# Performance work log

Hardware: AMD Instinct MI355X
Metric: run time of the kernel (lower is better)

## Reference

```python
import jax, jax.numpy as jnp
import numpy as np

H = 512  # hidden_size


def setup_inputs() -> dict:
    key = jax.random.key(0)
    ks = jax.random.split(key, 8)
    B, L_tgt, L_src = 4, 32, 1024
    query = jax.random.normal(ks[0], (B, L_tgt, H), dtype=jnp.float32)
    states = jax.random.normal(ks[1], (B, L_src, 2 * H), dtype=jnp.float32)
    source_mask = jnp.ones((B, L_src), dtype=jnp.int32)
    s = 0.02
    Wq = jax.random.normal(ks[2], (H, 2 * H), dtype=jnp.float32) * s      # _linear_query.weight^T
    bq = jax.random.normal(ks[3], (2 * H,), dtype=jnp.float32) * s        # _linear_query.bias
    Ws = jax.random.normal(ks[4], (2 * H, 2 * H), dtype=jnp.float32) * s  # _linear_source.weight^T (no bias)
    v = jax.random.normal(ks[5], (2 * H,), dtype=jnp.float32) * s         # _v.weight (no bias)
    Wc = jax.random.normal(ks[6], (3 * H, H), dtype=jnp.float32) * s      # _context.weight^T
    bc = jax.random.normal(ks[7], (H,), dtype=jnp.float32) * s            # _context.bias
    return {"query": query, "states": states, "source_mask": source_mask,
            "Wq": Wq, "bq": bq, "Ws": Ws, "v": v, "Wc": Wc, "bc": bc}


def reference(query, states, source_mask, Wq, bq, Ws, v, Wc, bc):
    # Bahdanau additive attention.
    # query: (B, T, H), states: (B, S, 2H), source_mask: (B, S)
    qf = query @ Wq + bq                         # (B, T, 2H)
    sf = states @ Ws                             # (B, S, 2H)
    # alignments: v . tanh(qf[:, :, None] + sf[:, None, :])  -> (B, T, S)
    feats = jnp.tanh(qf[:, :, None, :] + sf[:, None, :, :])  # (B, T, S, 2H)
    alignments = jnp.einsum('btsd,d->bts', feats, v)
    # mask (B, S) -> (B, 1, S); masked positions get -inf before softmax
    alignments = jnp.where(source_mask[:, None, :].astype(bool), alignments, -jnp.inf)
    attentions = jax.nn.softmax(alignments, axis=2)           # (B, T, S)
    context = jnp.einsum('bts,bsd->btd', attentions, states)  # (B, T, 2H)
    concat_context = jnp.concatenate((context, query), axis=2)  # (B, T, 3H)
    attention_hidden = concat_context @ Wc + bc               # (B, T, H)
    attentions_t = jnp.swapaxes(attentions, 1, 2)             # (B, S, T)
    return (context, attention_hidden, attentions_t)
```

## Files before the change

### kernel.cpp

```cpp
#include <hip/hip_runtime.h>
#include <math.h>


typedef unsigned short u16;
typedef __bf16 bf16x8 __attribute__((ext_vector_type(8)));
typedef float floatx4 __attribute__((ext_vector_type(4)));

#define B_ 4
#define T_ 32
#define S_ 1024
#define H_ 512
#define D_ 1024
#define BT_ 128
#define TWO_LOG2E 2.8853900817779268f
#define LOG2E 1.4426950408889634f

__device__ __forceinline__ float bf2f(u16 u) {
  unsigned int i = ((unsigned int)u) << 16;
  return __builtin_bit_cast(float, i);
}
__device__ __forceinline__ u16 f2bf(float f) {
  unsigned int i = __builtin_bit_cast(unsigned int, f);
  i += 0x7fffu + ((i >> 16) & 1u);
  return (u16)(i >> 16);
}
__device__ __forceinline__ void ld_g2l_16(const u16* g, u16* l) {
  __builtin_amdgcn_global_load_lds((__attribute__((address_space(1))) void*)(u16*)g,
                                   (__attribute__((address_space(3))) void*)l, 16, 0, 0);
}


__global__ __launch_bounds__(256) void prep_fused4(const float* __restrict__ states, const float* __restrict__ Ws,
                                                   const float* __restrict__ query, const float* __restrict__ Wq,
                                                   const float* __restrict__ bq,
                                                   u16* __restrict__ sbf, u16* __restrict__ sbfT,
                                                   u16* __restrict__ WsT, float* __restrict__ qfp,
                                                   float* __restrict__ rowsum) {
  __shared__ u16 tile[32][65];
  __shared__ float q[8][128];
  const int t = threadIdx.x;
  if (blockIdx.x < 512) {
    if (blockIdx.x == 0 && t < 128) rowsum[t] = 0.f;
    const int n0 = (blockIdx.x & 15) * 64, k0 = (blockIdx.x >> 4) * 32;
    const int kr = t >> 3, nc = (t & 7) * 8;
    const float* p = Ws + (size_t)(k0 + kr) * D_ + n0 + nc;
    float4 a = *(const float4*)p, b = *(const float4*)(p + 4);
    tile[kr][nc + 0] = f2bf(a.x); tile[kr][nc + 1] = f2bf(a.y);
    tile[kr][nc + 2] = f2bf(a.z); tile[kr][nc + 3] = f2bf(a.w);
    tile[kr][nc + 4] = f2bf(b.x); tile[kr][nc + 5] = f2bf(b.y);
    tile[kr][nc + 6] = f2bf(b.z); tile[kr][nc + 7] = f2bf(b.w);
    __syncthreads();
    const int nr = t >> 2, kc = (t & 3) * 8;
    union { uint4 v; u16 s[8]; } st;
#pragma unroll
    for (int i = 0; i < 8; ++i) st.s[i] = tile[kc + i][nr];
    *(uint4*)(WsT + (size_t)(n0 + nr) * D_ + k0 + kc) = st.v;
  } else if (blockIdx.x < 2560) {
    const int bid = blockIdx.x - 512;
    const int b = bid >> 9;
    const int r2 = bid & 511;
    const int d0 = (r2 & 15) * 64, s0 = (r2 >> 4) * 32;
    const int sr = t >> 3, dc = (t & 7) * 8;
    const float* p = states + ((size_t)b * S_ + s0 + sr) * D_ + d0 + dc;
    float4 a = *(const float4*)p, bb = *(const float4*)(p + 4);
    union { uint4 v; u16 s[8]; } pk;
    pk.s[0] = f2bf(a.x); pk.s[1] = f2bf(a.y); pk.s[2] = f2bf(a.z); pk.s[3] = f2bf(a.w);
    pk.s[4] = f2bf(bb.x); pk.s[5] = f2bf(bb.y); pk.s[6] = f2bf(bb.z); pk.s[7] = f2bf(bb.w);
    *(uint4*)(sbf + ((size_t)b * S_ + s0 + sr) * D_ + d0 + dc) = pk.v;
#pragma unroll
    for (int i = 0; i < 8; ++i) tile[sr][dc + i] = pk.s[i];
    __syncthreads();
    const int dr = t >> 2, sc = (t & 3) * 8;
    union { uint4 v; u16 s[8]; } st;
#pragma unroll
    for (int i = 0; i < 8; ++i) st.s[i] = tile[sc + i][dr];
    *(uint4*)(sbfT + ((size_t)b * D_ + d0 + dr) * S_ + s0 + sc) = st.v;
  } else {
    const int idx = blockIdx.x - 2560;
    const int c0 = (idx & 3) * 256, r0 = ((idx >> 2) & 15) * 8, ks = idx >> 6;
    const int k0 = ks * 128;
    for (int i = t; i < 8 * 128; i += 256) {
      const int rl = i >> 7, kk = i & 127;
      q[rl][kk] = query[(size_t)(r0 + rl) * H_ + k0 + kk];
    }
    __syncthreads();
    const int col = c0 + t;
    float acc[8] = {};
    for (int kk = 0; kk < 128; ++kk) {
      const float w = Wq[(size_t)(k0 + kk) * D_ + col];
#pragma unroll
      for (int r = 0; r < 8; ++r) acc[r] = fmaf(q[r][kk], w, acc[r]);
    }
    const float bb = (ks == 0) ? bq[col] : 0.f;
    float* dst = qfp + (size_t)ks * (BT_ * D_);
#pragma unroll
    for (int r = 0; r < 8; ++r)
      dst[(size_t)(r0 + r) * D_ + col] = TWO_LOG2E * (acc[r] + bb);
  }
}

__device__ __forceinline__ void f2f_stage(const u16* __restrict__ A, const u16* __restrict__ BT,
                                          u16* sAb, u16* sBb, int bm0, int bn0, int k0,
                                          int wv, int srow, int sp) {
#pragma unroll
  for (int j = 0; j < 4; ++j) {
    const int r = wv * 32 + j * 8 + srow;
    const int c = sp ^ (r & 7);
    ld_g2l_16(A + (size_t)(bm0 + r) * D_ + k0 + c * 8, sAb + (wv * 32 + j * 8) * 64);
  }
#pragma unroll
  for (int j = 0; j < 2; ++j) {
    const int r = wv * 16 + j * 8 + srow;
    const int c = sp ^ (r & 7);
    ld_g2l_16(BT + (size_t)(bn0 + r) * D_ + k0 + c * 8, sBb + (wv * 16 + j * 8) * 64);
  }
}

__device__ __forceinline__ void f2f_compute(const u16* sAb, const u16* sBb,
                                            int wm, int wn, int fm, int fq, floatx4 (&acc)[4][2]) {
#pragma unroll
  for (int win = 0; win < 2; ++win) {
    bf16x8 af[4], bfr[2];
#pragma unroll
    for (int i = 0; i < 4; ++i) {
      const int R = wm + i * 16 + fm;
      af[i] = *(const bf16x8*)&sAb[R * 64 + ((win * 4 + fq) ^ (R & 7)) * 8];
    }
#pragma unroll
    for (int j = 0; j < 2; ++j) {
      const int R = wn + j * 16 + fm;
      bfr[j] = *(const bf16x8*)&sBb[R * 64 + ((win * 4 + fq) ^ (R & 7)) * 8];
    }
#pragma unroll
    for (int i = 0; i < 4; ++i)
#pragma unroll
      for (int j = 0; j < 2; ++j)
        acc[i][j] = __builtin_amdgcn_mfma_f32_16x16x32_bf16(af[i], bfr[j], acc[i][j], 0, 0, 0);
  }
}

__global__ __launch_bounds__(256) void f2i_sfgemm(const u16* __restrict__ A, const u16* __restrict__ BT,
                                                  const float* __restrict__ qfp, float* __restrict__ Eq,
                                                  u16* __restrict__ Es) {
  __shared__ __align__(16) u16 sA[2][128 * 64];
  __shared__ __align__(16) u16 sB[2][64 * 64];
  const int bm0 = blockIdx.y * 128, bn0 = blockIdx.x * 64;
  const int t = threadIdx.x;
  const int wv = t >> 6, lane = t & 63;
  const int wm = (wv >> 1) * 64, wn = (wv & 1) * 32;
  const int fm = lane & 15, fq = lane >> 4;
  const int srow = lane >> 3, sp = lane & 7;

  {
    const int bid = blockIdx.y * 16 + blockIdx.x;
    const int idx = bid * 256 + t;
    const float s = qfp[idx] + qfp[BT_ * D_ + idx] +
                    qfp[2 * BT_ * D_ + idx] + qfp[3 * BT_ * D_ + idx];
    Eq[idx] = __builtin_amdgcn_exp2f(s);
  }

  floatx4 acc[4][2];
  const floatx4 fz = {0.f, 0.f, 0.f, 0.f};
#pragma unroll
  for (int i = 0; i < 4; ++i) { acc[i][0] = fz; acc[i][1] = fz; }

  f2f_stage(A, BT, sA[0], sB[0], bm0, bn0, 0, wv, srow, sp);
#pragma unroll 1
  for (int k0 = 0; k0 < D_; k0 += 128) {
    f2f_stage(A, BT, sA[1], sB[1], bm0, bn0, k0 + 64, wv, srow, sp);
    asm volatile("s_waitcnt vmcnt(6)" ::: "memory");
    __builtin_amdgcn_s_barrier();
    f2f_compute(sA[0], sB[0], wm, wn, fm, fq, acc);
    __builtin_amdgcn_s_barrier();
    if (k0 + 128 < D_) {
      f2f_stage(A, BT, sA[0], sB[0], bm0, bn0, k0 + 128, wv, srow, sp);
      asm volatile("s_waitcnt vmcnt(6)" ::: "memory");
    } else {
      asm volatile("s_waitcnt vmcnt(0)" ::: "memory");
    }
    __builtin_amdgcn_s_barrier();
    f2f_compute(sA[1], sB[1], wm, wn, fm, fq, acc);
    __builtin_amdgcn_s_barrier();
  }
#pragma unroll
  for (int i = 0; i < 4; ++i)
#pragma unroll
    for (int j = 0; j < 2; ++j)
#pragma unroll
      for (int r = 0; r < 4; ++r) {
        const int row = bm0 + wm + i * 16 + fq * 4 + r;
        const int col = bn0 + wn + j * 16 + fm;
        Es[(size_t)row * D_ + col] = f2bf(__builtin_amdgcn_exp2f(TWO_LOG2E * acc[i][j][r]));
      }
}

__global__ __launch_bounds__(256) void f3i_align(const float* __restrict__ Eq, const u16* __restrict__ Es,
                                                 const float* __restrict__ v, const int* __restrict__ mask,
                                                 u16* __restrict__ pbf, float* __restrict__ rowsum) {
  __shared__ float red[32][4];
  const int wid = (blockIdx.x * 256 + threadIdx.x) >> 6;
  const int lane = threadIdx.x & 63;
  const int wv = threadIdx.x >> 6;
  const int b = wid >> 10, s = wid & 1023;
  const int msk = mask[(size_t)b * S_ + s];
  float vm2[16], es[16];
  float sumv = 0.f;
  {
    union { uint4 u[2]; u16 h[16]; } ue;
    const uint4* ep = (const uint4*)(Es + (size_t)wid * D_ + lane * 16);
    ue.u[0] = ep[0]; ue.u[1] = ep[1];
    const float4* vp = (const float4*)(v + lane * 16);
#pragma unroll
    for (int c = 0; c < 4; ++c) {
      const float4 w4 = vp[c];
      vm2[4 * c + 0] = -2.f * w4.x; vm2[4 * c + 1] = -2.f * w4.y;
      vm2[4 * c + 2] = -2.f * w4.z; vm2[4 * c + 3] = -2.f * w4.w;
      sumv += w4.x + w4.y + w4.z + w4.w;
    }
#pragma unroll
    for (int j = 0; j < 16; ++j) es[j] = bf2f(ue.h[j]);
  }
  const float* qbase = Eq + ((size_t)(b * T_)) * D_ + lane * 16;
  for (int tc = 0; tc < 8; ++tc) {
    float sum[4];
#pragma unroll
    for (int ti = 0; ti < 4; ++ti) {
      const float4* qp = (const float4*)(qbase + (size_t)(tc * 4 + ti) * D_);
      float acc = sumv;
#pragma unroll
      for (int c = 0; c < 4; ++c) {
        const float4 q4 = qp[c];
        const float xs[4] = {q4.x, q4.y, q4.z, q4.w};
#pragma unroll
        for (int u2 = 0; u2 < 4; ++u2) {
          const int j = 4 * c + u2;
          acc = fmaf(vm2[j], __builtin_amdgcn_rcpf(fmaf(xs[u2], es[j], 1.f)), acc);
        }
      }
      sum[ti] = acc;
    }
#pragma unroll
    for (int off = 32; off > 0; off >>= 1)
#pragma unroll
      for (int ti = 0; ti < 4; ++ti) sum[ti] += __shfl_xor(sum[ti], off);
    if (lane == 0) {
#pragma unroll
      for (int ti = 0; ti < 4; ++ti) {
        const int tt = tc * 4 + ti;
        const float e = msk ? __builtin_amdgcn_exp2f(sum[ti] * LOG2E) : 0.f;
        const u16 pe = f2bf(e);
        pbf[((size_t)(b * T_ + tt)) * S_ + s] = pe;
        red[tt][wv] = bf2f(pe);
      }
    }
  }
  __syncthreads();
  if (threadIdx.x < 32) {
    const int bb = blockIdx.x >> 8;
    const float rs = red[threadIdx.x][0] + red[threadIdx.x][1] +
                     red[threadIdx.x][2] + red[threadIdx.x][3];
    atomicAdd(&rowsum[bb * 32 + threadIdx.x], rs);
  }
}

__global__ __launch_bounds__(256) void f5d_context(const u16* __restrict__ pbf, const u16* __restrict__ sbfT,
                                                   const float* __restrict__ rowsum,
                                                   float* __restrict__ ctx, float* __restrict__ out_at) {
  __shared__ float rinv[32];
  const int b = blockIdx.x >> 4, dt = blockIdx.x & 15;
  if (threadIdx.x < 32) rinv[threadIdx.x] = 1.f / rowsum[b * 32 + threadIdx.x];
  __syncthreads();
  const int wv = threadIdx.x >> 6, lane = threadIdx.x & 63;
  const int n0 = dt * 64 + wv * 16;
  const int fm = lane & 15, fq = lane >> 4;
  const floatx4 fz = {0.f, 0.f, 0.f, 0.f};
  floatx4 acc0 = fz, acc1 = fz;
  const u16* pa0 = pbf + ((size_t)b * T_ + fm) * S_ + fq * 8;
  const u16* pa1 = pbf + ((size_t)b * T_ + 16 + fm) * S_ + fq * 8;
  const u16* pb  = sbfT + ((size_t)b * D_ + n0 + fm) * S_ + fq * 8;
#pragma unroll 4
  for (int k0 = 0; k0 < S_; k0 += 32) {
    bf16x8 a0 = *(const bf16x8*)(pa0 + k0);
    bf16x8 a1 = *(const bf16x8*)(pa1 + k0);
    bf16x8 bb = *(const bf16x8*)(pb + k0);
    acc0 = __builtin_amdgcn_mfma_f32_16x16x32_bf16(a0, bb, acc0, 0, 0, 0);
    acc1 = __builtin_amdgcn_mfma_f32_16x16x32_bf16(a1, bb, acc1, 0, 0, 0);
  }
  const int col = n0 + fm;
#pragma unroll
  for (int r = 0; r < 4; ++r) {
    const int t0r = fq * 4 + r;
    ctx[((size_t)b * T_ + t0r) * D_ + col] = acc0[r] * rinv[t0r];
    ctx[((size_t)b * T_ + 16 + t0r) * D_ + col] = acc1[r] * rinv[16 + t0r];
  }
  const int s0 = dt * 64;
  for (int i = threadIdx.x; i < 64 * 32; i += 256) {
    const int tt = i >> 6, sl = i & 63;
    const float e = bf2f(pbf[((size_t)(b * T_ + tt)) * S_ + s0 + sl]);
    out_at[((size_t)(b * S_ + s0 + sl)) * T_ + tt] = e * rinv[tt];
  }
}

__global__ __launch_bounds__(256) void f6b_outproj(const float* __restrict__ ctx, const float* __restrict__ query,
                                                   const float* __restrict__ Wc, const float* __restrict__ bc,
                                                   float* __restrict__ out_hid) {
  __shared__ float cq[16][128];
  const int c0 = blockIdx.x * 128, r0 = blockIdx.y * 16, k0 = blockIdx.z * 128;
  const int tid = threadIdx.x;
  const int cl = tid & 127, rh = tid >> 7;
  for (int i = tid; i < 16 * 128; i += 256) {
    const int rl = i >> 7, kk = i & 127;
    const int k = k0 + kk, row = r0 + rl;
    cq[rl][kk] = (k < D_) ? ctx[(size_t)row * D_ + k] : query[(size_t)row * H_ + k - D_];
  }
  __syncthreads();
  float acc[8] = {};
  for (int kk = 0; kk < 128; ++kk) {
    const float w = Wc[(size_t)(k0 + kk) * H_ + c0 + cl];
#pragma unroll
    for (int rr = 0; rr < 8; ++rr) acc[rr] = fmaf(cq[rh * 8 + rr][kk], w, acc[rr]);
  }
  const float bb = (blockIdx.z == 0) ? bc[c0 + cl] : 0.f;
#pragma unroll
  for (int rr = 0; rr < 8; ++rr)
    atomicAdd(&out_hid[(size_t)(r0 + rh * 8 + rr) * H_ + c0 + cl], acc[rr] + bb);
}


__global__ __launch_bounds__(256) void prep_fused(const float* __restrict__ states, const float* __restrict__ Ws,
                                                  const float* __restrict__ query, const float* __restrict__ Wq,
                                                  const float* __restrict__ bq,
                                                  u16* __restrict__ sbf, u16* __restrict__ sbfT,
                                                  u16* __restrict__ WsT, float* __restrict__ qf) {
  __shared__ u16 tile[32][65];
  __shared__ float q[8][128];
  const int t = threadIdx.x;
  if (blockIdx.x < 512) {
    const int n0 = (blockIdx.x & 15) * 64, k0 = (blockIdx.x >> 4) * 32;
    const int kr = t >> 3, nc = (t & 7) * 8;
    const float* p = Ws + (size_t)(k0 + kr) * D_ + n0 + nc;
    float4 a = *(const float4*)p, b = *(const float4*)(p + 4);
    tile[kr][nc + 0] = f2bf(a.x); tile[kr][nc + 1] = f2bf(a.y);
    tile[kr][nc + 2] = f2bf(a.z); tile[kr][nc + 3] = f2bf(a.w);
    tile[kr][nc + 4] = f2bf(b.x); tile[kr][nc + 5] = f2bf(b.y);
    tile[kr][nc + 6] = f2bf(b.z); tile[kr][nc + 7] = f2bf(b.w);
    __syncthreads();
    const int nr = t >> 2, kc = (t & 3) * 8;
    union { uint4 v; u16 s[8]; } st;
#pragma unroll
    for (int i = 0; i < 8; ++i) st.s[i] = tile[kc + i][nr];
    *(uint4*)(WsT + (size_t)(n0 + nr) * D_ + k0 + kc) = st.v;
  } else if (blockIdx.x < 2560) {
    const int bid = blockIdx.x - 512;
    const int b = bid >> 9;
    const int r2 = bid & 511;
    const int d0 = (r2 & 15) * 64, s0 = (r2 >> 4) * 32;
    const int sr = t >> 3, dc = (t & 7) * 8;
    const float* p = states + ((size_t)b * S_ + s0 + sr) * D_ + d0 + dc;
    float4 a = *(const float4*)p, bb = *(const float4*)(p + 4);
    union { uint4 v; u16 s[8]; } pk;
    pk.s[0] = f2bf(a.x); pk.s[1] = f2bf(a.y); pk.s[2] = f2bf(a.z); pk.s[3] = f2bf(a.w);
    pk.s[4] = f2bf(bb.x); pk.s[5] = f2bf(bb.y); pk.s[6] = f2bf(bb.z); pk.s[7] = f2bf(bb.w);
    *(uint4*)(sbf + ((size_t)b * S_ + s0 + sr) * D_ + d0 + dc) = pk.v;
#pragma unroll
    for (int i = 0; i < 8; ++i) tile[sr][dc + i] = pk.s[i];
    __syncthreads();
    const int dr = t >> 2, sc = (t & 3) * 8;
    union { uint4 v; u16 s[8]; } st;
#pragma unroll
    for (int i = 0; i < 8; ++i) st.s[i] = tile[sc + i][dr];
    *(uint4*)(sbfT + ((size_t)b * D_ + d0 + dr) * S_ + s0 + sc) = st.v;
  } else {
    const int idx = blockIdx.x - 2560;
    const int c0 = (idx & 3) * 256, r0 = ((idx >> 2) & 15) * 8, k0 = (idx >> 6) * 128;
    for (int i = t; i < 8 * 128; i += 256) {
      const int rl = i >> 7, kk = i & 127;
      q[rl][kk] = query[(size_t)(r0 + rl) * H_ + k0 + kk];
    }
    __syncthreads();
    const int col = c0 + t;
    float acc[8] = {};
    for (int kk = 0; kk < 128; ++kk) {
      const float w = Wq[(size_t)(k0 + kk) * D_ + col];
#pragma unroll
      for (int r = 0; r < 8; ++r) acc[r] = fmaf(q[r][kk], w, acc[r]);
    }
    const float bb = (k0 == 0) ? bq[col] : 0.f;
#pragma unroll
    for (int r = 0; r < 8; ++r)
      atomicAdd(&qf[(size_t)(r0 + r) * D_ + col], TWO_LOG2E * (acc[r] + bb));
  }
}

__global__ __launch_bounds__(256) void f2e_sfgemm(const u16* __restrict__ A, const u16* __restrict__ BT,
                                                  u16* __restrict__ Cb) {
  __shared__ __align__(16) u16 sA[128 * 64];
  __shared__ __align__(16) u16 sB[64 * 64];
  const int bm0 = blockIdx.y * 128, bn0 = blockIdx.x * 64;
  const int t = threadIdx.x;
  const int wv = t >> 6, lane = t & 63;
  const int wm = (wv >> 1) * 64, wn = (wv & 1) * 32;
  const int fm = lane & 15, fq = lane >> 4;
  const int srow = lane >> 3, sp = lane & 7;

  floatx4 acc[4][2];
  const floatx4 fz = {0.f, 0.f, 0.f, 0.f};
#pragma unroll
  for (int i = 0; i < 4; ++i) { acc[i][0] = fz; acc[i][1] = fz; }

  for (int k0 = 0; k0 < D_; k0 += 64) {
    __syncthreads();
#pragma unroll
    for (int j = 0; j < 4; ++j) {
      const int r = wv * 32 + j * 8 + srow;
      const int c = sp ^ (r & 7);
      ld_g2l_16(A + (size_t)(bm0 + r) * D_ + k0 + c * 8, &sA[(wv * 32 + j * 8) * 64]);
    }
#pragma unroll
    for (int j = 0; j < 2; ++j) {
      const int r = wv * 16 + j * 8 + srow;
      const int c = sp ^ (r & 7);
      ld_g2l_16(BT + (size_t)(bn0 + r) * D_ + k0 + c * 8, &sB[(wv * 16 + j * 8) * 64]);
    }
    __syncthreads();
#pragma unroll
    for (int win = 0; win < 2; ++win) {
      bf16x8 af[4], bfr[2];
#pragma unroll
      for (int i = 0; i < 4; ++i) {
        const int R = wm + i * 16 + fm;
        af[i] = *(const bf16x8*)&sA[R * 64 + ((win * 4 + fq) ^ (R & 7)) * 8];
      }
#pragma unroll
      for (int j = 0; j < 2; ++j) {
        const int R = wn + j * 16 + fm;
        bfr[j] = *(const bf16x8*)&sB[R * 64 + ((win * 4 + fq) ^ (R & 7)) * 8];
      }
#pragma unroll
      for (int i = 0; i < 4; ++i)
#pragma unroll
        for (int j = 0; j < 2; ++j)
          acc[i][j] = __builtin_amdgcn_mfma_f32_16x16x32_bf16(af[i], bfr[j], acc[i][j], 0, 0, 0);
    }
  }
#pragma unroll
  for (int i = 0; i < 4; ++i)
#pragma unroll
    for (int j = 0; j < 2; ++j)
#pragma unroll
      for (int r = 0; r < 4; ++r) {
        const int row = bm0 + wm + i * 16 + fq * 4 + r;
        const int col = bn0 + wn + j * 16 + fm;
        Cb[(size_t)row * D_ + col] = f2bf(TWO_LOG2E * acc[i][j][r]);
      }
}

__global__ __launch_bounds__(256, 6) void f3f_align(const float* __restrict__ qf, const u16* __restrict__ sfb,
                                                    const float* __restrict__ v, float* __restrict__ alg) {
  const int wid = (blockIdx.x * 256 + threadIdx.x) >> 6;
  const int lane = threadIdx.x & 63;
  const int b = wid >> 10, s = wid & 1023;
  const int t0 = blockIdx.y * 16;
  float vr[16], sr[16];
  {
    union { uint4 v[2]; u16 s[16]; } u;
    const uint4* sp = (const uint4*)(sfb + (size_t)wid * D_ + lane * 16);
    u.v[0] = sp[0]; u.v[1] = sp[1];
    const float* vp = v + lane * 16;
#pragma unroll
    for (int c = 0; c < 4; ++c) {
      float4 w = *(const float4*)(vp + 4 * c);
      vr[4 * c + 0] = w.x; vr[4 * c + 1] = w.y; vr[4 * c + 2] = w.z; vr[4 * c + 3] = w.w;
    }
#pragma unroll
    for (int j = 0; j < 16; ++j) sr[j] = bf2f(u.s[j]);
  }
  float sum[16];
#pragma unroll
  for (int tt = 0; tt < 16; ++tt) sum[tt] = 0.f;

  const float* qbase = qf + ((size_t)(b * T_ + t0)) * D_ + lane * 16;
  for (int tt = 0; tt < 16; ++tt) {
    const float4* qp = (const float4*)(qbase + (size_t)tt * D_);
    float acc = 0.f;
#pragma unroll
    for (int c = 0; c < 4; ++c) {
      float4 q4 = qp[c];
      float xs[4] = {q4.x, q4.y, q4.z, q4.w};
#pragma unroll
      for (int u2 = 0; u2 < 4; ++u2) {
        const int j = 4 * c + u2;
        const float x = xs[u2] + sr[j];
        const float e = __builtin_amdgcn_exp2f(x);
        acc = fmaf(vr[j], fmaf(-2.f, __builtin_amdgcn_rcpf(e + 1.f), 1.f), acc);
      }
    }
    sum[tt] = acc;
  }
#pragma unroll
  for (int off = 32; off > 0; off >>= 1)
#pragma unroll
    for (int tt = 0; tt < 16; ++tt) sum[tt] += __shfl_xor(sum[tt], off);
  if (lane == 0) {
#pragma unroll
    for (int tt = 0; tt < 16; ++tt)
      alg[((size_t)(b * T_ + t0 + tt)) * S_ + s] = sum[tt];
  }
}

__global__ __launch_bounds__(256) void f4b_softmax(const float* __restrict__ alg, const int* __restrict__ mask,
                                                   float* __restrict__ out_at, u16* __restrict__ pbf) {
  const int r = blockIdx.x;
  const int b = r >> 5, t = r & 31;
  const int tid = threadIdx.x;
  __shared__ float red[256];
  float a[4];
#pragma unroll
  for (int jj = 0; jj < 4; ++jj) {
    const int s = tid + 256 * jj;
    const float x = alg[(size_t)r * S_ + s];
    a[jj] = (mask[(size_t)b * S_ + s] != 0) ? x : -3.0e38f;
  }
  float m = fmaxf(fmaxf(a[0], a[1]), fmaxf(a[2], a[3]));
  red[tid] = m; __syncthreads();
  for (int st = 128; st > 0; st >>= 1) { if (tid < st) red[tid] = fmaxf(red[tid], red[tid + st]); __syncthreads(); }
  m = red[0]; __syncthreads();
  float e[4], lsum = 0.f;
#pragma unroll
  for (int jj = 0; jj < 4; ++jj) {
    e[jj] = (a[jj] > -1.0e38f) ? expf(a[jj] - m) : 0.f;
    lsum += e[jj];
  }
  red[tid] = lsum; __syncthreads();
  for (int st = 128; st > 0; st >>= 1) { if (tid < st) red[tid] += red[tid + st]; __syncthreads(); }
  const float rs = 1.f / red[0];
#pragma unroll
  for (int jj = 0; jj < 4; ++jj) {
    const int s = tid + 256 * jj;
    const float p = e[jj] * rs;
    out_at[((size_t)b * S_ + s) * T_ + t] = p;
    pbf[(size_t)r * S_ + s] = f2bf(p);
  }
}

__global__ __launch_bounds__(256) void f5c_context(const u16* __restrict__ pbf, const u16* __restrict__ sbfT,
                                                   float* __restrict__ ctx) {
  const int b = blockIdx.x >> 4, dt = blockIdx.x & 15;
  const int wv = threadIdx.x >> 6, lane = threadIdx.x & 63;
  const int n0 = dt * 64 + wv * 16;
  const int fm = lane & 15, fq = lane >> 4;
  const floatx4 fz = {0.f, 0.f, 0.f, 0.f};
  floatx4 acc0 = fz, acc1 = fz;
  const u16* pa0 = pbf + ((size_t)b * T_ + fm) * S_ + fq * 8;
  const u16* pa1 = pbf + ((size_t)b * T_ + 16 + fm) * S_ + fq * 8;
  const u16* pb  = sbfT + ((size_t)b * D_ + n0 + fm) * S_ + fq * 8;
#pragma unroll 4
  for (int k0 = 0; k0 < S_; k0 += 32) {
    bf16x8 a0 = *(const bf16x8*)(pa0 + k0);
    bf16x8 a1 = *(const bf16x8*)(pa1 + k0);
    bf16x8 bb = *(const bf16x8*)(pb + k0);
    acc0 = __builtin_amdgcn_mfma_f32_16x16x32_bf16(a0, bb, acc0, 0, 0, 0);
    acc1 = __builtin_amdgcn_mfma_f32_16x16x32_bf16(a1, bb, acc1, 0, 0, 0);
  }
  const int col = n0 + fm;
#pragma unroll
  for (int r = 0; r < 4; ++r) {
    ctx[((size_t)b * T_ + fq * 4 + r) * D_ + col] = acc0[r];
    ctx[((size_t)b * T_ + 16 + fq * 4 + r) * D_ + col] = acc1[r];
  }
}


__global__ __launch_bounds__(256) void kc_cvt(const float* __restrict__ in, u16* __restrict__ out) {
  const size_t i0 = ((size_t)blockIdx.x * 256 + threadIdx.x) * 8;
  float4 a = *(const float4*)(in + i0);
  float4 b = *(const float4*)(in + i0 + 4);
  union { uint4 v; u16 s[8]; } r;
  r.s[0] = f2bf(a.x); r.s[1] = f2bf(a.y); r.s[2] = f2bf(a.z); r.s[3] = f2bf(a.w);
  r.s[4] = f2bf(b.x); r.s[5] = f2bf(b.y); r.s[6] = f2bf(b.z); r.s[7] = f2bf(b.w);
  *(uint4*)(out + i0) = r.v;
}

__global__ __launch_bounds__(256) void f0_transpose(const float* __restrict__ Ws, u16* __restrict__ WsT) {
  __shared__ u16 tile[32][65];
  const int n0 = blockIdx.x * 64, k0 = blockIdx.y * 32;
  const int t = threadIdx.x;
  {
    const int kr = t >> 3, nc = (t & 7) * 8;
    const float* p = Ws + (size_t)(k0 + kr) * D_ + n0 + nc;
    float4 a = *(const float4*)p, b = *(const float4*)(p + 4);
    tile[kr][nc + 0] = f2bf(a.x); tile[kr][nc + 1] = f2bf(a.y);
    tile[kr][nc + 2] = f2bf(a.z); tile[kr][nc + 3] = f2bf(a.w);
    tile[kr][nc + 4] = f2bf(b.x); tile[kr][nc + 5] = f2bf(b.y);
    tile[kr][nc + 6] = f2bf(b.z); tile[kr][nc + 7] = f2bf(b.w);
  }
  __syncthreads();
  {
    const int nr = t >> 2, kc = (t & 3) * 8;
    union { uint4 v; u16 s[8]; } st;
#pragma unroll
    for (int i = 0; i < 8; ++i) st.s[i] = tile[kc + i][nr];
    *(uint4*)(WsT + (size_t)(n0 + nr) * D_ + k0 + kc) = st.v;
  }
}

__global__ __launch_bounds__(256) void f1b_qf(const float* __restrict__ query, const float* __restrict__ Wq,
                                              const float* __restrict__ bq, float* __restrict__ qf) {
  __shared__ float q[8][128];
  const int c0 = blockIdx.x * 256, r0 = blockIdx.y * 8, k0 = blockIdx.z * 128;
  const int tid = threadIdx.x;
  for (int i = tid; i < 8 * 128; i += 256) {
    const int rl = i >> 7, kk = i & 127;
    q[rl][kk] = query[(size_t)(r0 + rl) * H_ + k0 + kk];
  }
  __syncthreads();
  const int col = c0 + tid;
  float acc[8] = {};
  for (int kk = 0; kk < 128; ++kk) {
    const float w = Wq[(size_t)(k0 + kk) * D_ + col];
#pragma unroll
    for (int r = 0; r < 8; ++r) acc[r] = fmaf(q[r][kk], w, acc[r]);
  }
  const float bb = (blockIdx.z == 0) ? bq[col] : 0.f;
#pragma unroll
  for (int r = 0; r < 8; ++r)
    atomicAdd(&qf[(size_t)(r0 + r) * D_ + col], TWO_LOG2E * (acc[r] + bb));
}

__global__ __launch_bounds__(256) void f2c_sfgemm(const u16* __restrict__ A, const u16* __restrict__ BT,
                                                  u16* __restrict__ Cb) {
  __shared__ __align__(16) u16 sA[128 * 40];
  __shared__ __align__(16) u16 sB[64 * 40];
  const int bm0 = blockIdx.y * 128, bn0 = blockIdx.x * 64;
  const int t = threadIdx.x;
  const int wv = t >> 6, lane = t & 63;
  const int wm = (wv >> 1) * 64, wn = (wv & 1) * 32;
  const int fm = lane & 15, fq = lane >> 4;
  const int arow = t >> 1, akc = (t & 1) * 16;
  const int brow = t >> 2, bkc = (t & 3) * 8;
  floatx4 acc[4][2];
  const floatx4 fz = {0.f, 0.f, 0.f, 0.f};
#pragma unroll
  for (int i = 0; i < 4; ++i) { acc[i][0] = fz; acc[i][1] = fz; }
  const uint4* gA = (const uint4*)(A + (size_t)(bm0 + arow) * D_ + akc);
  const uint4* gB = (const uint4*)(BT + (size_t)(bn0 + brow) * D_ + bkc);
  for (int k0 = 0; k0 < D_; k0 += 32) {
    uint4 va0 = gA[k0 >> 3];
    uint4 va1 = gA[(k0 >> 3) + 1];
    uint4 vb = gB[k0 >> 3];
    __syncthreads();
    *(uint4*)&sA[arow * 40 + akc] = va0;
    *(uint4*)&sA[arow * 40 + akc + 8] = va1;
    *(uint4*)&sB[brow * 40 + bkc] = vb;
    __syncthreads();
    bf16x8 af[4], bfr[2];
#pragma unroll
    for (int i = 0; i < 4; ++i) af[i] = *(const bf16x8*)&sA[(wm + i * 16 + fm) * 40 + fq * 8];
#pragma unroll
    for (int j = 0; j < 2; ++j) bfr[j] = *(const bf16x8*)&sB[(wn + j * 16 + fm) * 40 + fq * 8];
#pragma unroll
    for (int i = 0; i < 4; ++i)
#pragma unroll
      for (int j = 0; j < 2; ++j)
        acc[i][j] = __builtin_amdgcn_mfma_f32_16x16x32_bf16(af[i], bfr[j], acc[i][j], 0, 0, 0);
  }
#pragma unroll
  for (int i = 0; i < 4; ++i)
#pragma unroll
    for (int j = 0; j < 2; ++j)
#pragma unroll
      for (int r = 0; r < 4; ++r) {
        const int row = bm0 + wm + i * 16 + fq * 4 + r;
        const int col = bn0 + wn + j * 16 + fm;
        Cb[(size_t)row * D_ + col] = f2bf(TWO_LOG2E * acc[i][j][r]);
      }
}

__global__ __launch_bounds__(256) void f2d_sfgemm(const float* __restrict__ A, const u16* __restrict__ BT,
                                                  u16* __restrict__ Cb) {
  __shared__ __align__(16) u16 sA[128 * 40];
  __shared__ __align__(16) u16 sB[64 * 40];
  const int bm0 = blockIdx.y * 128, bn0 = blockIdx.x * 64;
  const int t = threadIdx.x;
  const int wv = t >> 6, lane = t & 63;
  const int wm = (wv >> 1) * 64, wn = (wv & 1) * 32;
  const int fm = lane & 15, fq = lane >> 4;
  const int arow = t >> 1, akc = (t & 1) * 16;
  const int brow = t >> 2, bkc = (t & 3) * 8;
  floatx4 acc[4][2];
  const floatx4 fz = {0.f, 0.f, 0.f, 0.f};
#pragma unroll
  for (int i = 0; i < 4; ++i) { acc[i][0] = fz; acc[i][1] = fz; }
  const float* gA = A + (size_t)(bm0 + arow) * D_ + akc;
  const uint4* gB = (const uint4*)(BT + (size_t)(bn0 + brow) * D_ + bkc);
  for (int k0 = 0; k0 < D_; k0 += 32) {
    float4 a0 = *(const float4*)(gA + k0);
    float4 a1 = *(const float4*)(gA + k0 + 4);
    float4 a2 = *(const float4*)(gA + k0 + 8);
    float4 a3 = *(const float4*)(gA + k0 + 12);
    uint4 vb = gB[k0 >> 3];
    union { uint4 v[2]; u16 s[16]; } pa;
    pa.s[0] = f2bf(a0.x); pa.s[1] = f2bf(a0.y); pa.s[2] = f2bf(a0.z); pa.s[3] = f2bf(a0.w);
    pa.s[4] = f2bf(a1.x); pa.s[5] = f2bf(a1.y); pa.s[6] = f2bf(a1.z); pa.s[7] = f2bf(a1.w);
    pa.s[8] = f2bf(a2.x); pa.s[9] = f2bf(a2.y); pa.s[10] = f2bf(a2.z); pa.s[11] = f2bf(a2.w);
    pa.s[12] = f2bf(a3.x); pa.s[13] = f2bf(a3.y); pa.s[14] = f2bf(a3.z); pa.s[15] = f2bf(a3.w);
    __syncthreads();
    *(uint4*)&sA[arow * 40 + akc] = pa.v[0];
    *(uint4*)&sA[arow * 40 + akc + 8] = pa.v[1];
    *(uint4*)&sB[brow * 40 + bkc] = vb;
    __syncthreads();
    bf16x8 af[4], bfr[2];
#pragma unroll
    for (int i = 0; i < 4; ++i) af[i] = *(const bf16x8*)&sA[(wm + i * 16 + fm) * 40 + fq * 8];
#pragma unroll
    for (int j = 0; j < 2; ++j) bfr[j] = *(const bf16x8*)&sB[(wn + j * 16 + fm) * 40 + fq * 8];
#pragma unroll
    for (int i = 0; i < 4; ++i)
#pragma unroll
      for (int j = 0; j < 2; ++j)
        acc[i][j] = __builtin_amdgcn_mfma_f32_16x16x32_bf16(af[i], bfr[j], acc[i][j], 0, 0, 0);
  }
#pragma unroll
  for (int i = 0; i < 4; ++i)
#pragma unroll
    for (int j = 0; j < 2; ++j)
#pragma unroll
      for (int r = 0; r < 4; ++r) {
        const int row = bm0 + wm + i * 16 + fq * 4 + r;
        const int col = bn0 + wn + j * 16 + fm;
        Cb[(size_t)row * D_ + col] = f2bf(TWO_LOG2E * acc[i][j][r]);
      }
}

__global__ __launch_bounds__(256) void f4_softmax(const float* __restrict__ alg, const int* __restrict__ mask,
                                                  float* __restrict__ attn) {
  const int r = blockIdx.x;
  const int b = r >> 5;
  const int tid = threadIdx.x;
  __shared__ float red[256];
  float a[4];
#pragma unroll
  for (int jj = 0; jj < 4; ++jj) {
    const int s = tid + 256 * jj;
    const float x = alg[(size_t)r * S_ + s];
    a[jj] = (mask[(size_t)b * S_ + s] != 0) ? x : -3.0e38f;
  }
  float m = fmaxf(fmaxf(a[0], a[1]), fmaxf(a[2], a[3]));
  red[tid] = m; __syncthreads();
  for (int st = 128; st > 0; st >>= 1) { if (tid < st) red[tid] = fmaxf(red[tid], red[tid + st]); __syncthreads(); }
  m = red[0]; __syncthreads();
  float e[4], lsum = 0.f;
#pragma unroll
  for (int jj = 0; jj < 4; ++jj) {
    e[jj] = (a[jj] > -1.0e38f) ? expf(a[jj] - m) : 0.f;
    lsum += e[jj];
  }
  red[tid] = lsum; __syncthreads();
  for (int st = 128; st > 0; st >>= 1) { if (tid < st) red[tid] += red[tid + st]; __syncthreads(); }
  const float rs = 1.f / red[0];
#pragma unroll
  for (int jj = 0; jj < 4; ++jj)
    attn[(size_t)r * S_ + tid + 256 * jj] = e[jj] * rs;
}

__global__ __launch_bounds__(256) void f5b_context(const float* __restrict__ attn, const u16* __restrict__ sbf,
                                                   float* __restrict__ ctx, float* __restrict__ out_at) {
  __shared__ float at[16][64];
  const int s0 = blockIdx.x * 64, t0 = blockIdx.y * 16, b = blockIdx.z;
  const int tid = threadIdx.x;
  for (int i = tid; i < 16 * 64; i += 256) {
    const int tl = i >> 6, sl = i & 63;
    at[tl][sl] = attn[(size_t)(b * T_ + t0 + tl) * S_ + s0 + sl];
  }
  __syncthreads();
  for (int i = tid; i < 64 * 16; i += 256) {
    const int sl = i >> 4, tl = i & 15;
    out_at[((size_t)b * S_ + s0 + sl) * T_ + t0 + tl] = at[tl][sl];
  }
  float acc[16][4] = {};
  for (int sl = 0; sl < 64; ++sl) {
    const u16* srow = sbf + ((size_t)b * S_ + s0 + sl) * D_ + tid;
    float sv[4];
#pragma unroll
    for (int jj = 0; jj < 4; ++jj) sv[jj] = bf2f(srow[256 * jj]);
#pragma unroll
    for (int tl = 0; tl < 16; ++tl) {
      const float w = at[tl][sl];
#pragma unroll
      for (int jj = 0; jj < 4; ++jj) acc[tl][jj] = fmaf(w, sv[jj], acc[tl][jj]);
    }
  }
#pragma unroll
  for (int tl = 0; tl < 16; ++tl)
#pragma unroll
    for (int jj = 0; jj < 4; ++jj)
      atomicAdd(&ctx[(size_t)(b * T_ + t0 + tl) * D_ + tid + 256 * jj], acc[tl][jj]);
}

__global__ __launch_bounds__(256) void f5_context(const float* __restrict__ attn, const float* __restrict__ states,
                                                  float* __restrict__ ctx, float* __restrict__ out_at) {
  __shared__ float at[16][64];
  const int s0 = blockIdx.x * 64, t0 = blockIdx.y * 16, b = blockIdx.z;
  const int tid = threadIdx.x;
  for (int i = tid; i < 16 * 64; i += 256) {
    const int tl = i >> 6, sl = i & 63;
    at[tl][sl] = attn[(size_t)(b * T_ + t0 + tl) * S_ + s0 + sl];
  }
  __syncthreads();
  for (int i = tid; i < 64 * 16; i += 256) {
    const int sl = i >> 4, tl = i & 15;
    out_at[((size_t)b * S_ + s0 + sl) * T_ + t0 + tl] = at[tl][sl];
  }
  float acc[16][4] = {};
  for (int sl = 0; sl < 64; ++sl) {
    const float* srow = states + ((size_t)b * S_ + s0 + sl) * D_ + tid;
    float sv[4];
#pragma unroll
    for (int jj = 0; jj < 4; ++jj) sv[jj] = srow[256 * jj];
#pragma unroll
    for (int tl = 0; tl < 16; ++tl) {
      const float w = at[tl][sl];
#pragma unroll
      for (int jj = 0; jj < 4; ++jj) acc[tl][jj] = fmaf(w, sv[jj], acc[tl][jj]);
    }
  }
#pragma unroll
  for (int tl = 0; tl < 16; ++tl)
#pragma unroll
    for (int jj = 0; jj < 4; ++jj)
      atomicAdd(&ctx[(size_t)(b * T_ + t0 + tl) * D_ + tid + 256 * jj], acc[tl][jj]);
}


__global__ __launch_bounds__(256) void k1_qf(const float* __restrict__ query, const float* __restrict__ Wq,
                                             const float* __restrict__ bq, float* __restrict__ qf) {
  const int r = blockIdx.x;
  const int tid = threadIdx.x;
  __shared__ float q[H_];
  for (int i = tid; i < H_; i += 256) q[i] = query[(size_t)r * H_ + i];
  __syncthreads();
#pragma unroll
  for (int jj = 0; jj < 4; ++jj) {
    const int j = tid + 256 * jj;
    float acc = bq[j];
    for (int k = 0; k < H_; ++k) acc = fmaf(q[k], Wq[(size_t)k * D_ + j], acc);
    qf[(size_t)r * D_ + j] = acc;
  }
}

__global__ __launch_bounds__(256) void k23_align(const float* __restrict__ states, const float* __restrict__ Ws,
                                                 const float* __restrict__ v, const float* __restrict__ qf,
                                                 float* __restrict__ alg) {
  const int b = blockIdx.x >> 6;
  const int s0 = (blockIdx.x & 63) * 16;
  const int tid = threadIdx.x, lane = tid & 63, wv = tid >> 6;
  __shared__ u16 stL[16 * D_];
  __shared__ float vvL[D_];
  __shared__ float red[16 * 4];
  for (int i = tid; i < 16 * D_; i += 256) {
    const int row = i >> 10, col = i & (D_ - 1);
    stL[i] = f2bf(states[((size_t)b * S_ + s0 + row) * D_ + col]);
  }
  for (int i = tid; i < D_; i += 256) vvL[i] = v[i];
  __syncthreads();
  float acc[64];
#pragma unroll
  for (int i = 0; i < 64; ++i) acc[i] = 0.f;
#pragma unroll 4
  for (int k = 0; k < D_; ++k) {
    float wsv[4];
#pragma unroll
    for (int jj = 0; jj < 4; ++jj) wsv[jj] = Ws[(size_t)k * D_ + tid + 256 * jj];
#pragma unroll
    for (int i = 0; i < 16; ++i) {
      const float sv = bf2f(stL[i * D_ + k]);
#pragma unroll
      for (int jj = 0; jj < 4; ++jj) acc[i * 4 + jj] = fmaf(sv, wsv[jj], acc[i * 4 + jj]);
    }
  }
  for (int t = 0; t < T_; ++t) {
    float qv[4];
#pragma unroll
    for (int jj = 0; jj < 4; ++jj) qv[jj] = qf[((size_t)b * T_ + t) * D_ + tid + 256 * jj];
    float part[16];
#pragma unroll
    for (int i = 0; i < 16; ++i) {
      float p = 0.f;
#pragma unroll
      for (int jj = 0; jj < 4; ++jj)
        p = fmaf(vvL[tid + 256 * jj], tanhf(qv[jj] + acc[i * 4 + jj]), p);
      part[i] = p;
    }
#pragma unroll
    for (int i = 0; i < 16; ++i) {
      float x = part[i];
#pragma unroll
      for (int off = 32; off > 0; off >>= 1) x += __shfl_xor(x, off);
      if (lane == 0) red[i * 4 + wv] = x;
    }
    __syncthreads();
    if (tid < 16)
      alg[((size_t)b * T_ + t) * S_ + s0 + tid] =
          red[tid * 4 + 0] + red[tid * 4 + 1] + red[tid * 4 + 2] + red[tid * 4 + 3];
    __syncthreads();
  }
}

__global__ __launch_bounds__(256) void k4_softmax(const float* __restrict__ alg, const int* __restrict__ mask,
                                                  float* __restrict__ attn) {
  const int r = blockIdx.x;
  const int b = r >> 5;
  const int tid = threadIdx.x;
  __shared__ float red[256];
  float a[4];
#pragma unroll
  for (int jj = 0; jj < 4; ++jj) {
    const int s = tid + 256 * jj;
    const float x = alg[(size_t)r * S_ + s];
    a[jj] = (mask[(size_t)b * S_ + s] != 0) ? x : -3.0e38f;
  }
  float m = fmaxf(fmaxf(a[0], a[1]), fmaxf(a[2], a[3]));
  red[tid] = m; __syncthreads();
  for (int st = 128; st > 0; st >>= 1) { if (tid < st) red[tid] = fmaxf(red[tid], red[tid + st]); __syncthreads(); }
  m = red[0]; __syncthreads();
  float e[4], lsum = 0.f;
#pragma unroll
  for (int jj = 0; jj < 4; ++jj) {
    e[jj] = (a[jj] > -1.0e38f) ? expf(a[jj] - m) : 0.f;
    lsum += e[jj];
  }
  red[tid] = lsum; __syncthreads();
  for (int st = 128; st > 0; st >>= 1) { if (tid < st) red[tid] += red[tid + st]; __syncthreads(); }
  const float rs = 1.f / red[0];
#pragma unroll
  for (int jj = 0; jj < 4; ++jj)
    attn[(size_t)r * S_ + tid + 256 * jj] = e[jj] * rs;
}

__global__ __launch_bounds__(256) void k56_ctx_proj(const float* __restrict__ attn, const float* __restrict__ states,
                                                    const float* __restrict__ query, const float* __restrict__ Wc,
                                                    const float* __restrict__ bc,
                                                    float* __restrict__ out_ctx, float* __restrict__ out_hid,
                                                    float* __restrict__ out_at) {
  const int r = blockIdx.x;
  const int b = r >> 5, t = r & (T_ - 1);
  const int tid = threadIdx.x;
  __shared__ float pr[S_];
  __shared__ float cq[D_ + H_];
  for (int s = tid; s < S_; s += 256) pr[s] = attn[(size_t)r * S_ + s];
  __syncthreads();
  for (int s = tid; s < S_; s += 256) out_at[((size_t)b * S_ + s) * T_ + t] = pr[s];
  float acc[4] = {0.f, 0.f, 0.f, 0.f};
  for (int s = 0; s < S_; ++s) {
    const float w = pr[s];
    const float* srow = states + ((size_t)b * S_ + s) * D_ + tid;
#pragma unroll
    for (int jj = 0; jj < 4; ++jj) acc[jj] = fmaf(w, srow[256 * jj], acc[jj]);
  }
#pragma unroll
  for (int jj = 0; jj < 4; ++jj) {
    cq[tid + 256 * jj] = acc[jj];
    out_ctx[(size_t)r * D_ + tid + 256 * jj] = acc[jj];
  }
  for (int i = tid; i < H_; i += 256) cq[D_ + i] = query[(size_t)r * H_ + i];
  __syncthreads();
#pragma unroll
  for (int jj = 0; jj < 2; ++jj) {
    const int n = tid + 256 * jj;
    float h = bc[n];
    for (int k = 0; k < D_ + H_; ++k) h = fmaf(cq[k], Wc[(size_t)k * H_ + n], h);
    out_hid[(size_t)r * H_ + n] = h;
  }
}

extern "C" void kernel_launch(void* const* d_in, const int* in_sizes, int n_in,
                              void* d_out, int out_size, void* d_ws, size_t ws_size,
                              hipStream_t stream) {
  const float* query  = (const float*)d_in[0];
  const float* states = (const float*)d_in[1];
  const int*   mask   = (const int*)d_in[2];
  const float* Wq     = (const float*)d_in[3];
  const float* bq     = (const float*)d_in[4];
  const float* Ws     = (const float*)d_in[5];
  const float* v      = (const float*)d_in[6];
  const float* Wc     = (const float*)d_in[7];
  const float* bc     = (const float*)d_in[8];

  float* A  = (float*)d_out;
  float* Bh = A + (size_t)BT_ * D_;
  float* C  = Bh + (size_t)BT_ * H_;

  char* ws = (char*)d_ws;
  u16*   sfb  = (u16*)(ws + 0);
  u16*   WsT  = (u16*)(ws + 8388608);
  float* alg  = (float*)(ws + 10485760);
  u16*   sbf  = (u16*)(ws + 11010048);
  u16*   sbfT = (u16*)(ws + 19398656);
  u16*   pbf  = (u16*)(ws + 27787264);

  const size_t WS_T1 = 11010048;
  const size_t WS_T2 = 19398656;
  const size_t WS_T3 = 28049408;
  const size_t WS_T4 = 36962816;

  if (ws_size >= WS_T4) {
    float* qfp  = (float*)(ws + 0);
    u16*   Es16 = (u16*)(ws + 28049408);
    float* Eq4  = (float*)(ws + 36438016);
    float* rsum = (float*)(ws + 36962304);
    (void)hipMemsetAsync(Bh, 0, (size_t)BT_ * H_ * 4, stream);
    prep_fused4<<<2816, 256, 0, stream>>>(states, Ws, query, Wq, bq, sbf, sbfT, WsT, qfp, rsum);
    f2i_sfgemm<<<dim3(16, 32), 256, 0, stream>>>(sbf, WsT, qfp, Eq4, Es16);
    f3i_align<<<1024, 256, 0, stream>>>(Eq4, Es16, v, mask, pbf, rsum);
    f5d_context<<<64, 256, 0, stream>>>(pbf, sbfT, rsum, A, C);
    f6b_outproj<<<dim3(4, 8, 12), 256, 0, stream>>>(A, query, Wc, bc, Bh);
  } else if (ws_size >= WS_T3) {
    (void)hipMemsetAsync(A, 0, (size_t)(BT_ * D_ + BT_ * H_) * 4, stream);
    prep_fused<<<2816, 256, 0, stream>>>(states, Ws, query, Wq, bq, sbf, sbfT, WsT, A);
    f2e_sfgemm<<<dim3(16, 32), 256, 0, stream>>>(sbf, WsT, sfb);
    f3f_align<<<dim3(1024, 2), 256, 0, stream>>>(A, sfb, v, alg);
    f4b_softmax<<<BT_, 256, 0, stream>>>(alg, mask, C, pbf);
    f5c_context<<<64, 256, 0, stream>>>(pbf, sbfT, A);
    f6b_outproj<<<dim3(4, 8, 12), 256, 0, stream>>>(A, query, Wc, bc, Bh);
  } else if (ws_size >= WS_T1) {
    float* attn = alg;
    (void)hipMemsetAsync(A, 0, (size_t)(BT_ * D_ + BT_ * H_) * 4, stream);
    f1b_qf<<<dim3(4, 16, 4), 256, 0, stream>>>(query, Wq, bq, A);
    f0_transpose<<<dim3(16, 32), 256, 0, stream>>>(Ws, WsT);
    const int tier2 = (ws_size >= WS_T2);
    if (tier2) {
      kc_cvt<<<2048, 256, 0, stream>>>(states, sbf);
      f2c_sfgemm<<<dim3(16, 32), 256, 0, stream>>>(sbf, WsT, sfb);
    } else {
      f2d_sfgemm<<<dim3(16, 32), 256, 0, stream>>>(states, WsT, sfb);
    }
    f3f_align<<<dim3(1024, 2), 256, 0, stream>>>(A, sfb, v, C);
    (void)hipMemsetAsync(A, 0, (size_t)BT_ * D_ * 4, stream);
    f4_softmax<<<BT_, 256, 0, stream>>>(C, mask, attn);
    if (tier2)
      f5b_context<<<dim3(16, 2, 4), 256, 0, stream>>>(attn, sbf, A, C);
    else
      f5_context<<<dim3(16, 2, 4), 256, 0, stream>>>(attn, states, A, C);
    f6b_outproj<<<dim3(4, 8, 12), 256, 0, stream>>>(A, query, Wc, bc, Bh);
  } else {
    k1_qf<<<BT_, 256, 0, stream>>>(query, Wq, bq, A);
    k23_align<<<B_ * (S_ / 16), 256, 0, stream>>>(states, Ws, v, A, C);
    k4_softmax<<<BT_, 256, 0, stream>>>(C, mask, A);
    k56_ctx_proj<<<BT_, 256, 0, stream>>>(A, states, query, Wc, bc, A, Bh, C);
  }
}
```

Before: 181.1 us.

## Fold query part of output projection into prep; process two sources per wave in align

The query-times-Wc slice of the output projection, plus its bias, moves into the prep kernel as 128 extra blocks that accumulate atomically into the hidden output. The final outproj kernel then covers only the context slice with a smaller grid. Separately, the alignment kernel now has each wave handle two source positions, so query loads and shuffle reductions are shared across both and pbf writes are packed pairs. The cost is more register pressure in the align kernel and half as many blocks.

```diff
diff --git a/kernel.cpp b/kernel.cpp
--- a/kernel.cpp
+++ b/kernel.cpp
@@ -30,12 +30,13 @@
 }
 
 
-__global__ __launch_bounds__(256) void prep_fused4(const float* __restrict__ states, const float* __restrict__ Ws,
+__global__ __launch_bounds__(256) void prep_fused5(const float* __restrict__ states, const float* __restrict__ Ws,
                                                    const float* __restrict__ query, const float* __restrict__ Wq,
                                                    const float* __restrict__ bq,
+                                                   const float* __restrict__ Wc, const float* __restrict__ bc,
                                                    u16* __restrict__ sbf, u16* __restrict__ sbfT,
                                                    u16* __restrict__ WsT, float* __restrict__ qfp,
-                                                   float* __restrict__ rowsum) {
+                                                   float* __restrict__ rowsum, float* __restrict__ hid) {
   __shared__ u16 tile[32][65];
   __shared__ float q[8][128];
   const int t = threadIdx.x;
@@ -75,7 +76,7 @@
 #pragma unroll
     for (int i = 0; i < 8; ++i) st.s[i] = tile[sc + i][dr];
     *(uint4*)(sbfT + ((size_t)b * D_ + d0 + dr) * S_ + s0 + sc) = st.v;
-  } else {
+  } else if (blockIdx.x < 2816) {
     const int idx = blockIdx.x - 2560;
     const int c0 = (idx & 3) * 256, r0 = ((idx >> 2) & 15) * 8, ks = idx >> 6;
     const int k0 = ks * 128;
@@ -96,6 +97,26 @@
 #pragma unroll
     for (int r = 0; r < 8; ++r)
       dst[(size_t)(r0 + r) * D_ + col] = TWO_LOG2E * (acc[r] + bb);
+  } else {
+    const int idx = blockIdx.x - 2816;
+    const int c0 = (idx & 1) * 256, r0 = ((idx >> 1) & 15) * 8, ks = idx >> 5;
+    const int k0 = ks * 128;
+    for (int i = t; i < 8 * 128; i += 256) {
+      const int rl = i >> 7, kk = i & 127;
+      q[rl][kk] = query[(size_t)(r0 + rl) * H_ + k0 + kk];
+    }
+    __syncthreads();
+    const int col = c0 + t;
+    float acc[8] = {};
+    for (int kk = 0; kk < 128; ++kk) {
+      const float w = Wc[(size_t)(D_ + k0 + kk) * H_ + col];
+#pragma unroll
+      for (int r = 0; r < 8; ++r) acc[r] = fmaf(q[r][kk], w, acc[r]);
+    }
+    const float bb = (ks == 0) ? bc[col] : 0.f;
+#pragma unroll
+    for (int r = 0; r < 8; ++r)
+      atomicAdd(&hid[(size_t)(r0 + r) * H_ + col], acc[r] + bb);
   }
 }
 
@@ -194,21 +215,25 @@
       }
 }
 
-__global__ __launch_bounds__(256) void f3i_align(const float* __restrict__ Eq, const u16* __restrict__ Es,
+__global__ __launch_bounds__(256) void f3j_align(const float* __restrict__ Eq, const u16* __restrict__ Es,
                                                  const float* __restrict__ v, const int* __restrict__ mask,
                                                  u16* __restrict__ pbf, float* __restrict__ rowsum) {
   __shared__ float red[32][4];
-  const int wid = (blockIdx.x * 256 + threadIdx.x) >> 6;
+  const int w = (blockIdx.x * 256 + threadIdx.x) >> 6;
   const int lane = threadIdx.x & 63;
   const int wv = threadIdx.x >> 6;
-  const int b = wid >> 10, s = wid & 1023;
-  const int msk = mask[(size_t)b * S_ + s];
-  float vm2[16], es[16];
+  const int b = w >> 9;
+  const int s0 = (w & 511) * 2;
+  const int msk0 = mask[(size_t)b * S_ + s0];
+  const int msk1 = mask[(size_t)b * S_ + s0 + 1];
+  float vm2[16], es0[16], es1[16];
   float sumv = 0.f;
   {
-    union { uint4 u[2]; u16 h[16]; } ue;
-    const uint4* ep = (const uint4*)(Es + (size_t)wid * D_ + lane * 16);
-    ue.u[0] = ep[0]; ue.u[1] = ep[1];
+    union { uint4 u[2]; u16 h[16]; } ua, ub;
+    const uint4* ep0 = (const uint4*)(Es + ((size_t)b * S_ + s0) * D_ + lane * 16);
+    const uint4* ep1 = (const uint4*)(Es + ((size_t)b * S_ + s0 + 1) * D_ + lane * 16);
+    ua.u[0] = ep0[0]; ua.u[1] = ep0[1];
+    ub.u[0] = ep1[0]; ub.u[1] = ep1[1];
     const float4* vp = (const float4*)(v + lane * 16);
 #pragma unroll
     for (int c = 0; c < 4; ++c) {
@@ -218,15 +243,15 @@
       sumv += w4.x + w4.y + w4.z + w4.w;
     }
 #pragma unroll
-    for (int j = 0; j < 16; ++j) es[j] = bf2f(ue.h[j]);
+    for (int j = 0; j < 16; ++j) { es0[j] = bf2f(ua.h[j]); es1[j] = bf2f(ub.h[j]); }
   }
   const float* qbase = Eq + ((size_t)(b * T_)) * D_ + lane * 16;
   for (int tc = 0; tc < 8; ++tc) {
-    float sum[4];
+    float sa[4], sb[4];
 #pragma unroll
     for (int ti = 0; ti < 4; ++ti) {
       const float4* qp = (const float4*)(qbase + (size_t)(tc * 4 + ti) * D_);
-      float acc = sumv;
+      float a0 = sumv, a1 = sumv;
 #pragma unroll
       for (int c = 0; c < 4; ++c) {
         const float4 q4 = qp[c];
@@ -234,29 +259,35 @@
 #pragma unroll
         for (int u2 = 0; u2 < 4; ++u2) {
           const int j = 4 * c + u2;
-          acc = fmaf(vm2[j], __builtin_amdgcn_rcpf(fmaf(xs[u2], es[j], 1.f)), acc);
+          a0 = fmaf(vm2[j], __builtin_amdgcn_rcpf(fmaf(xs[u2], es0[j], 1.f)), a0);
+          a1 = fmaf(vm2[j], __builtin_amdgcn_rcpf(fmaf(xs[u2], es1[j], 1.f)), a1);
         }
       }
-      sum[ti] = acc;
+      sa[ti] = a0; sb[ti] = a1;
     }
 #pragma unroll
     for (int off = 32; off > 0; off >>= 1)
 #pragma unroll
-      for (int ti = 0; ti < 4; ++ti) sum[ti] += __shfl_xor(sum[ti], off);
+      for (int ti = 0; ti < 4; ++ti) {
+        sa[ti] += __shfl_xor(sa[ti], off);
+        sb[ti] += __shfl_xor(sb[ti], off);
+      }
     if (lane == 0) {
 #pragma unroll
       for (int ti = 0; ti < 4; ++ti) {
         const int tt = tc * 4 + ti;
-        const float e = msk ? __builtin_amdgcn_exp2f(sum[ti] * LOG2E) : 0.f;
-        const u16 pe = f2bf(e);
-        pbf[((size_t)(b * T_ + tt)) * S_ + s] = pe;
-        red[tt][wv] = bf2f(pe);
+        const float e0 = msk0 ? __builtin_amdgcn_exp2f(sa[ti] * LOG2E) : 0.f;
+        const float e1 = msk1 ? __builtin_amdgcn_exp2f(sb[ti] * LOG2E) : 0.f;
+        const u16 p0 = f2bf(e0), p1 = f2bf(e1);
+        *(unsigned int*)&pbf[((size_t)(b * T_ + tt)) * S_ + s0] =
+            (unsigned int)p0 | ((unsigned int)p1 << 16);
+        red[tt][wv] = bf2f(p0) + bf2f(p1);
       }
     }
   }
   __syncthreads();
   if (threadIdx.x < 32) {
-    const int bb = blockIdx.x >> 8;
+    const int bb = blockIdx.x >> 7;
     const float rs = red[threadIdx.x][0] + red[threadIdx.x][1] +
                      red[threadIdx.x][2] + red[threadIdx.x][3];
     atomicAdd(&rowsum[bb * 32 + threadIdx.x], rs);
@@ -301,8 +332,8 @@
   }
 }
 
-__global__ __launch_bounds__(256) void f6b_outproj(const float* __restrict__ ctx, const float* __restrict__ query,
-                                                   const float* __restrict__ Wc, const float* __restrict__ bc,
+__global__ __launch_bounds__(256) void f6c_outproj(const float* __restrict__ ctx,
+                                                   const float* __restrict__ Wc,
                                                    float* __restrict__ out_hid) {
   __shared__ float cq[16][128];
   const int c0 = blockIdx.x * 128, r0 = blockIdx.y * 16, k0 = blockIdx.z * 128;
@@ -310,8 +341,7 @@
   const int cl = tid & 127, rh = tid >> 7;
   for (int i = tid; i < 16 * 128; i += 256) {
     const int rl = i >> 7, kk = i & 127;
-    const int k = k0 + kk, row = r0 + rl;
-    cq[rl][kk] = (k < D_) ? ctx[(size_t)row * D_ + k] : query[(size_t)row * H_ + k - D_];
+    cq[rl][kk] = ctx[(size_t)(r0 + rl) * D_ + k0 + kk];
   }
   __syncthreads();
   float acc[8] = {};
@@ -320,10 +350,9 @@
 #pragma unroll
     for (int rr = 0; rr < 8; ++rr) acc[rr] = fmaf(cq[rh * 8 + rr][kk], w, acc[rr]);
   }
-  const float bb = (blockIdx.z == 0) ? bc[c0 + cl] : 0.f;
 #pragma unroll
   for (int rr = 0; rr < 8; ++rr)
-    atomicAdd(&out_hid[(size_t)(r0 + rh * 8 + rr) * H_ + c0 + cl], acc[rr] + bb);
+    atomicAdd(&out_hid[(size_t)(r0 + rh * 8 + rr) * H_ + c0 + cl], acc[rr]);
 }
 
 
@@ -570,6 +599,31 @@
   }
 }
 
+__global__ __launch_bounds__(256) void f6b_outproj(const float* __restrict__ ctx, const float* __restrict__ query,
+                                                   const float* __restrict__ Wc, const float* __restrict__ bc,
+                                                   float* __restrict__ out_hid) {
+  __shared__ float cq[16][128];
+  const int c0 = blockIdx.x * 128, r0 = blockIdx.y * 16, k0 = blockIdx.z * 128;
+  const int tid = threadIdx.x;
+  const int cl = tid & 127, rh = tid >> 7;
+  for (int i = tid; i < 16 * 128; i += 256) {
+    const int rl = i >> 7, kk = i & 127;
+    const int k = k0 + kk, row = r0 + rl;
+    cq[rl][kk] = (k < D_) ? ctx[(size_t)row * D_ + k] : query[(size_t)row * H_ + k - D_];
+  }
+  __syncthreads();
+  float acc[8] = {};
+  for (int kk = 0; kk < 128; ++kk) {
+    const float w = Wc[(size_t)(k0 + kk) * H_ + c0 + cl];
+#pragma unroll
+    for (int rr = 0; rr < 8; ++rr) acc[rr] = fmaf(cq[rh * 8 + rr][kk], w, acc[rr]);
+  }
+  const float bb = (blockIdx.z == 0) ? bc[c0 + cl] : 0.f;
+#pragma unroll
+  for (int rr = 0; rr < 8; ++rr)
+    atomicAdd(&out_hid[(size_t)(r0 + rh * 8 + rr) * H_ + c0 + cl], acc[rr] + bb);
+}
+
 
 __global__ __launch_bounds__(256) void kc_cvt(const float* __restrict__ in, u16* __restrict__ out) {
   const size_t i0 = ((size_t)blockIdx.x * 256 + threadIdx.x) * 8;
@@ -1009,11 +1063,12 @@
     float* Eq4  = (float*)(ws + 36438016);
     float* rsum = (float*)(ws + 36962304);
     (void)hipMemsetAsync(Bh, 0, (size_t)BT_ * H_ * 4, stream);
-    prep_fused4<<<2816, 256, 0, stream>>>(states, Ws, query, Wq, bq, sbf, sbfT, WsT, qfp, rsum);
+    prep_fused5<<<2944, 256, 0, stream>>>(states, Ws, query, Wq, bq, Wc, bc,
+                                          sbf, sbfT, WsT, qfp, rsum, Bh);
     f2i_sfgemm<<<dim3(16, 32), 256, 0, stream>>>(sbf, WsT, qfp, Eq4, Es16);
-    f3i_align<<<1024, 256, 0, stream>>>(Eq4, Es16, v, mask, pbf, rsum);
+    f3j_align<<<512, 256, 0, stream>>>(Eq4, Es16, v, mask, pbf, rsum);
     f5d_context<<<64, 256, 0, stream>>>(pbf, sbfT, rsum, A, C);
-    f6b_outproj<<<dim3(4, 8, 12), 256, 0, stream>>>(A, query, Wc, bc, Bh);
+    f6c_outproj<<<dim3(4, 8, 8), 256, 0, stream>>>(A, Wc, Bh);
   } else if (ws_size >= WS_T3) {
     (void)hipMemsetAsync(A, 0, (size_t)(BT_ * D_ + BT_ * H_) * 4, stream);
     prep_fused<<<2816, 256, 0, stream>>>(states, Ws, query, Wq, bq, sbf, sbfT, WsT, A);
```

New measurement: 171.9 us. -5.1%, faster.
